# Optimization experiments

Hardware: AMD Instinct MI355X
Metric: run time of the kernel (lower is better)

Reference implementation:

```python
import jax, jax.numpy as jnp
import numpy as np

B, N = 8, 256
D_EQUI, D_INV, N_HEADS = 64, 256, 16
D_HEAD = D_INV // N_HEADS


def adj_to_attn_mask(adj):
    """0 where connected, -inf where not; fully-disconnected rows -> all 0."""
    adj_b = adj.astype(bool)
    mask = jnp.where(adj_b, jnp.float32(0.0), jnp.float32(-jnp.inf))
    row_any = adj_b.any(axis=-1, keepdims=True)
    return jnp.where(row_any, mask, jnp.float32(0.0))


def setup_inputs() -> dict:
    key = jax.random.key(0)
    ks = jax.random.split(key, 12)
    s = 0.05
    return {
        "v_equi": jax.random.normal(ks[0], (B, N, 3, D_EQUI), jnp.float32),
        "v_inv": jax.random.normal(ks[1], (B, N, D_INV), jnp.float32),
        "equi_messages": jax.random.normal(ks[2], (B, N, N, D_EQUI), jnp.float32),
        "inv_messages": jax.random.normal(ks[3], (B, N, N, N_HEADS), jnp.float32),
        "adj_mask": jax.random.randint(ks[4], (B, N, N), 0, 2, jnp.int32),
        "W_coord": jax.random.normal(ks[5], (D_EQUI, D_EQUI), jnp.float32) * s,
        "W_equi_out": jax.random.normal(ks[6], (D_EQUI, D_EQUI), jnp.float32) * s,
        "b_equi_out": jax.random.normal(ks[7], (D_EQUI,), jnp.float32) * s,
        "W_in": jax.random.normal(ks[8], (D_INV, D_INV), jnp.float32) * s,
        "b_in": jax.random.normal(ks[9], (D_INV,), jnp.float32) * s,
        "W_out": jax.random.normal(ks[10], (D_INV, D_INV), jnp.float32) * s,
        "b_out": jax.random.normal(ks[11], (D_INV,), jnp.float32) * s,
    }


def reference(v_equi, v_inv, equi_messages, inv_messages, adj_mask,
              W_coord, W_equi_out, b_equi_out, W_in, b_in, W_out, b_out):
    mask = adj_to_attn_mask(adj_mask)  # [B,Nq,Nkv]

    # ---- _EquiAttention ----
    # coord_proj (no bias): Linear over last dim d_equi (torch: x @ W.T)
    proj_equi = jnp.einsum('bkdc,oc->bkdo', v_equi, W_coord)          # [B,Nkv,3,C]
    attn_e = jax.nn.softmax(equi_messages + mask[..., None], axis=2)  # [B,Nq,Nkv,C]
    # per-channel bmm: (movedim/flatten/bmm) == einsum over kv per channel c
    out_e = jnp.einsum('bqkc,bkdc->bqdc', attn_e, proj_equi)          # [B,Nq,3,C]
    w_e = jnp.sqrt(jnp.sum(attn_e ** 2, axis=2))                      # [B,Nq,C]
    out_e = out_e * w_e[:, :, None, :]
    equi_updates = jnp.einsum('bqdc,oc->bqdo', out_e, W_equi_out) + b_equi_out

    # ---- _InvAttention ----
    attn_i = jax.nn.softmax(inv_messages + mask[..., None], axis=2)   # [B,Nq,Nkv,H]
    proj = jnp.einsum('bki,oi->bko', v_inv, W_in) + b_in              # [B,Nkv,d_inv]
    head_feats = proj.reshape(proj.shape[0], proj.shape[1], N_HEADS, D_HEAD)
    out_i = jnp.einsum('bqkh,bkhe->bqhe', attn_i, head_feats)         # [B,Nq,H,d_head]
    w_i = jnp.sqrt(jnp.sum(attn_i ** 2, axis=2))                      # [B,Nq,H]
    out_i = out_i * w_i[..., None]
    out_i = out_i.reshape(out_i.shape[0], out_i.shape[1], -1)         # [B,Nq,d_inv]
    inv_updates = jnp.einsum('bqi,oi->bqo', out_i, W_out) + b_out

    return (equi_updates, inv_updates)
```

## Files before the change

kernel.cpp:

```cpp
#include <hip/hip_runtime.h>
#include <hip/hip_bf16.h>
#include <stdint.h>

typedef unsigned short u16;

#define NINF (-__builtin_huge_valf())

__device__ __forceinline__ float bf2f(u16 h) {
    return __uint_as_float(((unsigned int)h) << 16);
}
__device__ __forceinline__ u16 f2bf(float f) {
    unsigned int u = __float_as_uint(f);
    u += 0x7FFFu + ((u >> 16) & 1u);
    return (u16)(u >> 16);
}
__device__ __forceinline__ void unpack8(uint4 u, float* f) {
    f[0] = __uint_as_float(u.x << 16);
    f[1] = __uint_as_float(u.x & 0xFFFF0000u);
    f[2] = __uint_as_float(u.y << 16);
    f[3] = __uint_as_float(u.y & 0xFFFF0000u);
    f[4] = __uint_as_float(u.z << 16);
    f[5] = __uint_as_float(u.z & 0xFFFF0000u);
    f[6] = __uint_as_float(u.w << 16);
    f[7] = __uint_as_float(u.w & 0xFFFF0000u);
}
__device__ __forceinline__ void unpack4(uint2 u, float* f) {
    f[0] = __uint_as_float(u.x << 16);
    f[1] = __uint_as_float(u.x & 0xFFFF0000u);
    f[2] = __uint_as_float(u.y << 16);
    f[3] = __uint_as_float(u.y & 0xFFFF0000u);
}

__global__ __launch_bounds__(192) void k_proj_equi(
    const float* __restrict__ v_equi,
    const float* __restrict__ W_coord,
    u16* __restrict__ proj)
{
    int bk = blockIdx.x;
    int t = threadIdx.x;
    __shared__ float vs[192];
    vs[t] = v_equi[(size_t)bk * 192 + t];
    __syncthreads();
    int d = t >> 6, o = t & 63;
    float acc = 0.f;
    const float* wrow = W_coord + o * 64;
#pragma unroll
    for (int c = 0; c < 64; c += 4) {
        float4 w = *(const float4*)(wrow + c);
        acc += vs[d * 64 + c + 0] * w.x;
        acc += vs[d * 64 + c + 1] * w.y;
        acc += vs[d * 64 + c + 2] * w.z;
        acc += vs[d * 64 + c + 3] * w.w;
    }
    proj[(size_t)bk * 192 + t] = f2bf(acc);
}

__global__ __launch_bounds__(256) void k_rowgemm_tobf16(
    const float* __restrict__ X,
    const float* __restrict__ W,
    const float* __restrict__ bias,
    u16* __restrict__ Y)
{
    int r0 = blockIdx.x * 8;
    int t = threadIdx.x;
    __shared__ float Xs[8][256];
#pragma unroll
    for (int i = 0; i < 8; ++i)
        Xs[i][t] = X[(size_t)(r0 + i) * 256 + t];
    __syncthreads();
    float acc[8];
    float bv = bias[t];
#pragma unroll
    for (int r = 0; r < 8; ++r) acc[r] = bv;
    const float* wrow = W + t * 256;
    for (int i = 0; i < 256; i += 4) {
        float4 w = *(const float4*)(wrow + i);
#pragma unroll
        for (int r = 0; r < 8; ++r) {
            acc[r] += Xs[r][i + 0] * w.x;
            acc[r] += Xs[r][i + 1] * w.y;
            acc[r] += Xs[r][i + 2] * w.z;
            acc[r] += Xs[r][i + 3] * w.w;
        }
    }
#pragma unroll
    for (int r = 0; r < 8; ++r)
        Y[(size_t)(r0 + r) * 256 + t] = f2bf(acc[r]);
}

__global__ __launch_bounds__(256) void k_rowgemm_tof32(
    const float* __restrict__ X,
    const float* __restrict__ W,
    const float* __restrict__ bias,
    float* __restrict__ Y)
{
    int r0 = blockIdx.x * 8;
    int t = threadIdx.x;
    __shared__ float Xs[8][256];
#pragma unroll
    for (int i = 0; i < 8; ++i)
        Xs[i][t] = X[(size_t)(r0 + i) * 256 + t];
    __syncthreads();
    float acc[8];
    float bv = bias[t];
#pragma unroll
    for (int r = 0; r < 8; ++r) acc[r] = bv;
    const float* wrow = W + t * 256;
    for (int i = 0; i < 256; i += 4) {
        float4 w = *(const float4*)(wrow + i);
#pragma unroll
        for (int r = 0; r < 8; ++r) {
            acc[r] += Xs[r][i + 0] * w.x;
            acc[r] += Xs[r][i + 1] * w.y;
            acc[r] += Xs[r][i + 2] * w.z;
            acc[r] += Xs[r][i + 3] * w.w;
        }
    }
#pragma unroll
    for (int r = 0; r < 8; ++r)
        Y[(size_t)(r0 + r) * 256 + t] = acc[r];
}

__global__ __launch_bounds__(256) void k_equi_attn(
    const float* __restrict__ equi_msg,
    const int* __restrict__ adj,
    const u16* __restrict__ proj,
    const float* __restrict__ W_eo,
    const float* __restrict__ b_eo,
    float* __restrict__ out)
{
    int bq = blockIdx.x;
    int b = bq >> 8;
    int t = threadIdx.x;

    __shared__ float maskv[256];
    __shared__ int anyflag;
    __shared__ float part[32][195];
    __shared__ float red_s[64], red_s2[64];
    __shared__ float out_s[3][64];

    if (t == 0) anyflag = 0;
    __syncthreads();
    int a = adj[(size_t)bq * 256 + t];
    if (a != 0) anyflag = 1;
    __syncthreads();
    maskv[t] = (a == 0 && anyflag != 0) ? NINF : 0.0f;
    __syncthreads();

    int kk = t >> 3;
    int c0 = (t & 7) * 8;
    float s[8], s2[8], a0[8], a1[8], a2[8];
#pragma unroll
    for (int u = 0; u < 8; ++u) { s[u] = 0.f; s2[u] = 0.f; a0[u] = 0.f; a1[u] = 0.f; a2[u] = 0.f; }

    const float* msg_base = equi_msg + (size_t)bq * 256 * 64;
    const u16* proj_base = proj + (size_t)b * 256 * 192;

#pragma unroll 4
    for (int j = 0; j < 8; ++j) {
        int k = kk + 32 * j;
        float m = maskv[k];
        float4 m0 = *(const float4*)(msg_base + k * 64 + c0);
        float4 m1 = *(const float4*)(msg_base + k * 64 + c0 + 4);
        const u16* pb = proj_base + k * 192 + c0;
        uint4 up0 = *(const uint4*)(pb);
        uint4 up1 = *(const uint4*)(pb + 64);
        uint4 up2 = *(const uint4*)(pb + 128);
        float mv[8], p0[8], p1[8], p2[8];
        mv[0] = m0.x; mv[1] = m0.y; mv[2] = m0.z; mv[3] = m0.w;
        mv[4] = m1.x; mv[5] = m1.y; mv[6] = m1.z; mv[7] = m1.w;
        unpack8(up0, p0); unpack8(up1, p1); unpack8(up2, p2);
#pragma unroll
        for (int u = 0; u < 8; ++u) {
            float e = __expf(mv[u] + m);
            s[u] += e;
            s2[u] += e * e;
            a0[u] += e * p0[u];
            a1[u] += e * p1[u];
            a2[u] += e * p2[u];
        }
    }

#pragma unroll
    for (int u = 0; u < 8; ++u) {
        part[kk][c0 + u] = s[u];
        part[kk][65 + c0 + u] = s2[u];
    }
    __syncthreads();
    if (t < 128) {
        int qq = t >> 6, c = t & 63;
        float sum = 0.f;
#pragma unroll
        for (int x = 0; x < 32; ++x) sum += part[x][qq * 65 + c];
        if (qq == 0) red_s[c] = sum; else red_s2[c] = sum;
    }
    __syncthreads();
#pragma unroll
    for (int u = 0; u < 8; ++u) {
        part[kk][c0 + u] = a0[u];
        part[kk][65 + c0 + u] = a1[u];
        part[kk][130 + c0 + u] = a2[u];
    }
    __syncthreads();
    if (t < 192) {
        int d = t >> 6, c = t & 63;
        float sum = 0.f;
#pragma unroll
        for (int x = 0; x < 32; ++x) sum += part[x][d * 65 + c];
        float sv = red_s[c];
        float scale = sqrtf(red_s2[c]) / (sv * sv);
        out_s[d][c] = sum * scale;
    }
    __syncthreads();
    if (t < 192) {
        int d = t >> 6, o = t & 63;
        float acc = b_eo[o];
        const float* wr = W_eo + o * 64;
#pragma unroll
        for (int c4 = 0; c4 < 64; c4 += 4) {
            float4 w = *(const float4*)(wr + c4);
            acc += out_s[d][c4 + 0] * w.x;
            acc += out_s[d][c4 + 1] * w.y;
            acc += out_s[d][c4 + 2] * w.z;
            acc += out_s[d][c4 + 3] * w.w;
        }
        out[(size_t)bq * 192 + t] = acc;
    }
}

__global__ __launch_bounds__(256) void k_inv_attn(
    const float* __restrict__ inv_msg,
    const int* __restrict__ adj,
    const u16* __restrict__ proj,
    float* __restrict__ out_rows)
{
    int bq = blockIdx.x;
    int b = bq >> 8;
    int t = threadIdx.x;

    __shared__ float maskv[256];
    __shared__ int anyflag;
    __shared__ float p_s[256][16];
    __shared__ float spart[16][16], s2part[16][16];
    __shared__ float sh_s[16], sh_s2[16];
    __shared__ float red[4][256];

    if (t == 0) anyflag = 0;
    __syncthreads();
    int a = adj[(size_t)bq * 256 + t];
    if (a != 0) anyflag = 1;
    __syncthreads();
    maskv[t] = (a == 0 && anyflag != 0) ? NINF : 0.0f;
    __syncthreads();

    {
        int h = t & 15, kk = t >> 4;
        float ss = 0.f, ss2 = 0.f;
        const float* mb = inv_msg + (size_t)bq * 256 * 16;
#pragma unroll
        for (int j = 0; j < 16; ++j) {
            int k = kk + 16 * j;
            float e = __expf(mb[k * 16 + h] + maskv[k]);
            p_s[k][h] = e;
            ss += e;
            ss2 += e * e;
        }
        spart[kk][h] = ss;
        s2part[kk][h] = ss2;
    }
    __syncthreads();
    if (t < 32) {
        int h = t & 15;
        float sum = 0.f;
        if (t < 16) {
#pragma unroll
            for (int kk = 0; kk < 16; ++kk) sum += spart[kk][h];
            sh_s[h] = sum;
        } else {
#pragma unroll
            for (int kk = 0; kk < 16; ++kk) sum += s2part[kk][h];
            sh_s2[h] = sum;
        }
    }
    __syncthreads();

    {
        int kk2 = t >> 6, h = (t >> 2) & 15, eg = t & 3;
        float acc[4] = {0.f, 0.f, 0.f, 0.f};
        const u16* pb = proj + (size_t)b * 256 * 256 + h * 16 + eg * 4;
        for (int j = 0; j < 64; ++j) {
            int k = kk2 + 4 * j;
            float p = p_s[k][h];
            uint2 u = *(const uint2*)(pb + k * 256);
            float w[4]; unpack4(u, w);
            acc[0] += p * w[0];
            acc[1] += p * w[1];
            acc[2] += p * w[2];
            acc[3] += p * w[3];
        }
#pragma unroll
        for (int ii = 0; ii < 4; ++ii) red[kk2][h * 16 + eg * 4 + ii] = acc[ii];
    }
    __syncthreads();
    {
        float sum = red[0][t] + red[1][t] + red[2][t] + red[3][t];
        int h = t >> 4;
        float sv = sh_s[h];
        out_rows[(size_t)bq * 256 + t] = sum * sqrtf(sh_s2[h]) / (sv * sv);
    }
}

extern "C" void kernel_launch(void* const* d_in, const int* in_sizes, int n_in,
                              void* d_out, int out_size, void* d_ws, size_t ws_size,
                              hipStream_t stream) {
    (void)in_sizes; (void)n_in; (void)out_size; (void)ws_size;

    const float* v_equi   = (const float*)d_in[0];
    const float* v_inv    = (const float*)d_in[1];
    const float* equi_msg = (const float*)d_in[2];
    const float* inv_msg  = (const float*)d_in[3];
    const int*   adj      = (const int*)d_in[4];
    const float* W_coord  = (const float*)d_in[5];
    const float* W_eo     = (const float*)d_in[6];
    const float* b_eo     = (const float*)d_in[7];
    const float* W_in     = (const float*)d_in[8];
    const float* b_in     = (const float*)d_in[9];
    const float* W_out    = (const float*)d_in[10];
    const float* b_out    = (const float*)d_in[11];
    float* out = (float*)d_out;

    char* ws = (char*)d_ws;
    u16*   proj_equi = (u16*)(ws);
    u16*   proj_inv  = (u16*)(ws + 786432);
    float* out_rows  = (float*)(ws + 786432 + 1048576);

    k_proj_equi<<<dim3(2048), dim3(192), 0, stream>>>(v_equi, W_coord, proj_equi);
    k_rowgemm_tobf16<<<dim3(256), dim3(256), 0, stream>>>(v_inv, W_in, b_in, proj_inv);
    k_equi_attn<<<dim3(2048), dim3(256), 0, stream>>>(equi_msg, adj, proj_equi, W_eo, b_eo, out);
    k_inv_attn<<<dim3(2048), dim3(256), 0, stream>>>(inv_msg, adj, proj_inv, out_rows);
    k_rowgemm_tof32<<<dim3(256), dim3(256), 0, stream>>>(out_rows, W_out, b_out, out + 393216);
}
```

Before: 313.8 us.

## Merge projection prologue kernels and process two query rows per inv-attention block

The two projection kernels are combined into one launch: the first 256 blocks do the v_inv projection, and 384 blocks each project 16 rows of v_equi into proj_equi. The inverse-attention kernel now handles two query rows per block, so each bf16 projection value it loads is used for both rows and the grid is halved. This targets launch overhead and repeated global reads of proj_inv. In exchange it uses more shared memory and registers per block, which may lower occupancy.

After: 291.8 us. 1.08x faster.

```diff
diff --git a/kernel.cpp b/kernel.cpp
--- a/kernel.cpp
+++ b/kernel.cpp
@@ -31,61 +31,66 @@
     f[3] = __uint_as_float(u.y & 0xFFFF0000u);
 }
 
-__global__ __launch_bounds__(192) void k_proj_equi(
+__global__ __launch_bounds__(256) void k_prologue(
+    const float* __restrict__ v_inv,
+    const float* __restrict__ W_in,
+    const float* __restrict__ b_in,
+    u16* __restrict__ proj_inv,
     const float* __restrict__ v_equi,
     const float* __restrict__ W_coord,
-    u16* __restrict__ proj)
+    u16* __restrict__ proj_equi)
 {
-    int bk = blockIdx.x;
-    int t = threadIdx.x;
-    __shared__ float vs[192];
-    vs[t] = v_equi[(size_t)bk * 192 + t];
-    __syncthreads();
-    int d = t >> 6, o = t & 63;
-    float acc = 0.f;
-    const float* wrow = W_coord + o * 64;
-#pragma unroll
-    for (int c = 0; c < 64; c += 4) {
-        float4 w = *(const float4*)(wrow + c);
-        acc += vs[d * 64 + c + 0] * w.x;
-        acc += vs[d * 64 + c + 1] * w.y;
-        acc += vs[d * 64 + c + 2] * w.z;
-        acc += vs[d * 64 + c + 3] * w.w;
-    }
-    proj[(size_t)bk * 192 + t] = f2bf(acc);
-}
-
-__global__ __launch_bounds__(256) void k_rowgemm_tobf16(
-    const float* __restrict__ X,
-    const float* __restrict__ W,
-    const float* __restrict__ bias,
-    u16* __restrict__ Y)
-{
-    int r0 = blockIdx.x * 8;
     int t = threadIdx.x;
     __shared__ float Xs[8][256];
-#pragma unroll
-    for (int i = 0; i < 8; ++i)
-        Xs[i][t] = X[(size_t)(r0 + i) * 256 + t];
-    __syncthreads();
-    float acc[8];
-    float bv = bias[t];
-#pragma unroll
-    for (int r = 0; r < 8; ++r) acc[r] = bv;
-    const float* wrow = W + t * 256;
-    for (int i = 0; i < 256; i += 4) {
-        float4 w = *(const float4*)(wrow + i);
-#pragma unroll
-        for (int r = 0; r < 8; ++r) {
-            acc[r] += Xs[r][i + 0] * w.x;
-            acc[r] += Xs[r][i + 1] * w.y;
-            acc[r] += Xs[r][i + 2] * w.z;
-            acc[r] += Xs[r][i + 3] * w.w;
-        }
-    }
-#pragma unroll
-    for (int r = 0; r < 8; ++r)
-        Y[(size_t)(r0 + r) * 256 + t] = f2bf(acc[r]);
+    __shared__ float Es[16][64];
+
+    if (blockIdx.x < 256) {
+        int r0 = blockIdx.x * 8;
+#pragma unroll
+        for (int i = 0; i < 8; ++i)
+            Xs[i][t] = v_inv[(size_t)(r0 + i) * 256 + t];
+        __syncthreads();
+        float acc[8];
+        float bv = b_in[t];
+#pragma unroll
+        for (int r = 0; r < 8; ++r) acc[r] = bv;
+        const float* wrow = W_in + t * 256;
+        for (int i = 0; i < 256; i += 4) {
+            float4 w = *(const float4*)(wrow + i);
+#pragma unroll
+            for (int r = 0; r < 8; ++r) {
+                acc[r] += Xs[r][i + 0] * w.x;
+                acc[r] += Xs[r][i + 1] * w.y;
+                acc[r] += Xs[r][i + 2] * w.z;
+                acc[r] += Xs[r][i + 3] * w.w;
+            }
+        }
+#pragma unroll
+        for (int r = 0; r < 8; ++r)
+            proj_inv[(size_t)(r0 + r) * 256 + t] = f2bf(acc[r]);
+    } else {
+        int bi = blockIdx.x - 256;
+        const float* src = v_equi + (size_t)bi * 1024;
+        ((float4*)Es)[t] = *(const float4*)(src + t * 4);
+        __syncthreads();
+        int o = t & 63, rr = t >> 6;
+        float acc[4] = {0.f, 0.f, 0.f, 0.f};
+        const float* wrow = W_coord + o * 64;
+#pragma unroll
+        for (int c = 0; c < 64; c += 4) {
+            float4 w = *(const float4*)(wrow + c);
+#pragma unroll
+            for (int m = 0; m < 4; ++m) {
+                int r = rr + 4 * m;
+                acc[m] += Es[r][c + 0] * w.x + Es[r][c + 1] * w.y
+                        + Es[r][c + 2] * w.z + Es[r][c + 3] * w.w;
+            }
+        }
+        u16* dst = proj_equi + (size_t)bi * 1024;
+#pragma unroll
+        for (int m = 0; m < 4; ++m)
+            dst[(rr + 4 * m) * 64 + o] = f2bf(acc[m]);
+    }
 }
 
 __global__ __launch_bounds__(256) void k_rowgemm_tof32(
@@ -228,85 +233,99 @@
     }
 }
 
-__global__ __launch_bounds__(256) void k_inv_attn(
+__global__ __launch_bounds__(256) void k_inv_attn2(
     const float* __restrict__ inv_msg,
     const int* __restrict__ adj,
     const u16* __restrict__ proj,
     float* __restrict__ out_rows)
 {
-    int bq = blockIdx.x;
-    int b = bq >> 8;
+    int bq2 = blockIdx.x;
+    int b = bq2 >> 7;
     int t = threadIdx.x;
 
-    __shared__ float maskv[256];
-    __shared__ int anyflag;
-    __shared__ float p_s[256][16];
-    __shared__ float spart[16][16], s2part[16][16];
-    __shared__ float sh_s[16], sh_s2[16];
-    __shared__ float red[4][256];
-
-    if (t == 0) anyflag = 0;
-    __syncthreads();
-    int a = adj[(size_t)bq * 256 + t];
-    if (a != 0) anyflag = 1;
-    __syncthreads();
-    maskv[t] = (a == 0 && anyflag != 0) ? NINF : 0.0f;
+    __shared__ float maskv[2][256];
+    __shared__ int anyflag[2];
+    __shared__ float p_s[2][256][16];
+    __shared__ float spart[2][16][16], s2part[2][16][16];
+    __shared__ float sh_s[2][16], sh_s2[2][16];
+    __shared__ float red[4][2][256];
+
+    if (t < 2) anyflag[t] = 0;
+    __syncthreads();
+    int a0 = adj[((size_t)bq2 * 2 + 0) * 256 + t];
+    int a1 = adj[((size_t)bq2 * 2 + 1) * 256 + t];
+    if (a0 != 0) anyflag[0] = 1;
+    if (a1 != 0) anyflag[1] = 1;
+    __syncthreads();
+    maskv[0][t] = (a0 == 0 && anyflag[0] != 0) ? NINF : 0.0f;
+    maskv[1][t] = (a1 == 0 && anyflag[1] != 0) ? NINF : 0.0f;
     __syncthreads();
 
     {
         int h = t & 15, kk = t >> 4;
-        float ss = 0.f, ss2 = 0.f;
-        const float* mb = inv_msg + (size_t)bq * 256 * 16;
-#pragma unroll
-        for (int j = 0; j < 16; ++j) {
-            int k = kk + 16 * j;
-            float e = __expf(mb[k * 16 + h] + maskv[k]);
-            p_s[k][h] = e;
-            ss += e;
-            ss2 += e * e;
-        }
-        spart[kk][h] = ss;
-        s2part[kk][h] = ss2;
-    }
-    __syncthreads();
-    if (t < 32) {
-        int h = t & 15;
+#pragma unroll
+        for (int q = 0; q < 2; ++q) {
+            const float* mb = inv_msg + ((size_t)bq2 * 2 + q) * 4096;
+            float ss = 0.f, ss2 = 0.f;
+#pragma unroll
+            for (int j = 0; j < 16; ++j) {
+                int k = kk + 16 * j;
+                float e = __expf(mb[k * 16 + h] + maskv[q][k]);
+                p_s[q][k][h] = e;
+                ss += e; ss2 += e * e;
+            }
+            spart[q][kk][h] = ss;
+            s2part[q][kk][h] = ss2;
+        }
+    }
+    __syncthreads();
+    if (t < 64) {
+        int q = t >> 5, sel = (t >> 4) & 1, h = t & 15;
         float sum = 0.f;
-        if (t < 16) {
-#pragma unroll
-            for (int kk = 0; kk < 16; ++kk) sum += spart[kk][h];
-            sh_s[h] = sum;
+        if (sel == 0) {
+#pragma unroll
+            for (int kk = 0; kk < 16; ++kk) sum += spart[q][kk][h];
+            sh_s[q][h] = sum;
         } else {
 #pragma unroll
-            for (int kk = 0; kk < 16; ++kk) sum += s2part[kk][h];
-            sh_s2[h] = sum;
+            for (int kk = 0; kk < 16; ++kk) sum += s2part[q][kk][h];
+            sh_s2[q][h] = sum;
         }
     }
     __syncthreads();
 
     {
         int kk2 = t >> 6, h = (t >> 2) & 15, eg = t & 3;
-        float acc[4] = {0.f, 0.f, 0.f, 0.f};
-        const u16* pb = proj + (size_t)b * 256 * 256 + h * 16 + eg * 4;
+        float acc0[4] = {0.f, 0.f, 0.f, 0.f};
+        float acc1[4] = {0.f, 0.f, 0.f, 0.f};
+        const u16* pb = proj + (size_t)b * 65536 + h * 16 + eg * 4;
         for (int j = 0; j < 64; ++j) {
             int k = kk2 + 4 * j;
-            float p = p_s[k][h];
-            uint2 u = *(const uint2*)(pb + k * 256);
+            uint2 u = *(const uint2*)(pb + (size_t)k * 256);
             float w[4]; unpack4(u, w);
-            acc[0] += p * w[0];
-            acc[1] += p * w[1];
-            acc[2] += p * w[2];
-            acc[3] += p * w[3];
-        }
-#pragma unroll
-        for (int ii = 0; ii < 4; ++ii) red[kk2][h * 16 + eg * 4 + ii] = acc[ii];
+            float pq0 = p_s[0][k][h];
+            float pq1 = p_s[1][k][h];
+#pragma unroll
+            for (int ii = 0; ii < 4; ++ii) {
+                acc0[ii] += pq0 * w[ii];
+                acc1[ii] += pq1 * w[ii];
+            }
+        }
+#pragma unroll
+        for (int ii = 0; ii < 4; ++ii) {
+            red[kk2][0][h * 16 + eg * 4 + ii] = acc0[ii];
+            red[kk2][1][h * 16 + eg * 4 + ii] = acc1[ii];
+        }
     }
     __syncthreads();
     {
-        float sum = red[0][t] + red[1][t] + red[2][t] + red[3][t];
         int h = t >> 4;
-        float sv = sh_s[h];
-        out_rows[(size_t)bq * 256 + t] = sum * sqrtf(sh_s2[h]) / (sv * sv);
+#pragma unroll
+        for (int q = 0; q < 2; ++q) {
+            float sum = red[0][q][t] + red[1][q][t] + red[2][q][t] + red[3][q][t];
+            float sv = sh_s[q][h];
+            out_rows[((size_t)bq2 * 2 + q) * 256 + t] = sum * sqrtf(sh_s2[q][h]) / (sv * sv);
+        }
     }
 }
 
@@ -334,9 +353,12 @@
     u16*   proj_inv  = (u16*)(ws + 786432);
     float* out_rows  = (float*)(ws + 786432 + 1048576);
 
-    k_proj_equi<<<dim3(2048), dim3(192), 0, stream>>>(v_equi, W_coord, proj_equi);
-    k_rowgemm_tobf16<<<dim3(256), dim3(256), 0, stream>>>(v_inv, W_in, b_in, proj_inv);
-    k_equi_attn<<<dim3(2048), dim3(256), 0, stream>>>(equi_msg, adj, proj_equi, W_eo, b_eo, out);
-    k_inv_attn<<<dim3(2048), dim3(256), 0, stream>>>(inv_msg, adj, proj_inv, out_rows);
-    k_rowgemm_tof32<<<dim3(256), dim3(256), 0, stream>>>(out_rows, W_out, b_out, out + 393216);
-}
+    k_prologue<<<dim3(640), dim3(256), 0, stream>>>(
+        v_inv, W_in, b_in, proj_inv, v_equi, W_coord, proj_equi);
+    k_equi_attn<<<dim3(2048), dim3(256), 0, stream>>>(
+        equi_msg, adj, proj_equi, W_eo, b_eo, out);
+    k_inv_attn2<<<dim3(1024), dim3(256), 0, stream>>>(
+        inv_msg, adj, proj_inv, out_rows);
+    k_rowgemm_tof32<<<dim3(256), dim3(256), 0, stream>>>(
+        out_rows, W_out, b_out, out + 393216);
+}
```
